# Optimization experiments

Measured on AMD Instinct MI355X. Metric: run time of the kernel, lower is better.

The kernel has to match this reference:

```python
import jax, jax.numpy as jnp
import numpy as np

N, E = 50000, 800000
F_N, F_E = 32, 16
HC, H, C, L = 128, 2, 64, 3  # hidden_channels, heads, out per head, num_layers
NEG_SLOPE = 0.2  # PyG GATConv default


def setup_inputs() -> dict:
    key = jax.random.key(0)
    ks = jax.random.split(key, 32)
    rn = lambda k, shape, s=0.05: (jax.random.normal(k, shape, jnp.float32) * s)
    return {
        "x": jax.random.normal(ks[0], (N, F_N), jnp.float32),
        "edge_index": jax.random.randint(ks[1], (2, E), 0, N),
        "edge_attr": jax.random.normal(ks[2], (E, F_E), jnp.float32),
        # node encoder: Linear(32,128) -> ReLU -> Linear(128,128)
        "w_n1": rn(ks[3], (F_N, HC)), "b_n1": jnp.zeros((HC,), jnp.float32),
        "w_n2": rn(ks[4], (HC, HC)), "b_n2": jnp.zeros((HC,), jnp.float32),
        # edge encoder: Linear(16,128) -> ReLU (output is ignored by GATConv, edge_dim=None)
        "w_e": rn(ks[5], (F_E, HC)), "b_e": jnp.zeros((HC,), jnp.float32),
        # 3 GATConv layers: lin [128,H*C], att_src/att_dst [H,C], bias [H*C]
        "conv_w": rn(ks[6], (L, HC, H * C)),
        "conv_att_src": rn(ks[7], (L, H, C)),
        "conv_att_dst": rn(ks[8], (L, H, C)),
        "conv_b": jnp.zeros((L, H * C), jnp.float32),
        # path prediction head: Linear(256,128)->ReLU->Linear(128,64)->ReLU->Linear(64,1)->Sigmoid
        "wp1": rn(ks[9], (2 * HC, HC)), "bp1": jnp.zeros((HC,), jnp.float32),
        "wp2": rn(ks[10], (HC, 64)), "bp2": jnp.zeros((64,), jnp.float32),
        "wp3": rn(ks[11], (64, 1)), "bp3": jnp.zeros((1,), jnp.float32),
        # vulnerability head: Linear(128,64)->ReLU->Linear(64,1)->Sigmoid
        "wv1": rn(ks[12], (HC, 64)), "bv1": jnp.zeros((64,), jnp.float32),
        "wv2": rn(ks[13], (64, 1)), "bv2": jnp.zeros((1,), jnp.float32),
    }


def _gat_layer(x, src, dst, w, att_src, att_dst, bias):
    n = x.shape[0]
    h = (x @ w).reshape(n, H, C)                       # [N,H,C]
    a_src = jnp.sum(h * att_src, axis=-1)              # [N,H]
    a_dst = jnp.sum(h * att_dst, axis=-1)              # [N,H]
    alpha = a_src[src] + a_dst[dst]                    # [E',H]
    alpha = jax.nn.leaky_relu(alpha, NEG_SLOPE)
    amax = jax.lax.stop_gradient(jax.ops.segment_max(alpha, dst, num_segments=n))
    ex = jnp.exp(alpha - amax[dst])
    denom = jax.ops.segment_sum(ex, dst, num_segments=n)  # [N,H] (>0: self-loops)
    coef = ex / denom[dst]                             # softmax over incoming edges
    msg = h[src] * coef[:, :, None]                    # [E',H,C]
    out = jax.ops.segment_sum(msg, dst, num_segments=n)
    return out.reshape(n, H * C) + bias


def reference(x, edge_index, edge_attr,
              w_n1, b_n1, w_n2, b_n2, w_e, b_e,
              conv_w, conv_att_src, conv_att_dst, conv_b,
              wp1, bp1, wp2, bp2, wp3, bp3, wv1, bv1, wv2, bv2):
    n = x.shape[0]
    # node encoder (dropout = identity in eval)
    h = jax.nn.relu(x @ w_n1 + b_n1) @ w_n2 + b_n2
    # edge encoder output is computed but ignored by GATConv (edge_dim=None in PyG)
    _edge_emb = jax.nn.relu(edge_attr @ w_e + b_e)
    # add self loops (GATConv default add_self_loops=True)
    loop = jnp.arange(n, dtype=edge_index.dtype)
    src = jnp.concatenate([edge_index[0], loop])
    dst = jnp.concatenate([edge_index[1], loop])
    for l in range(L):
        h = jax.nn.relu(_gat_layer(h, src, dst, conv_w[l], conv_att_src[l], conv_att_dst[l], conv_b[l]))
    g = jnp.mean(h, axis=0, keepdims=True)             # [1,128] graph embedding
    # path head on cat(x[:1], graph_embedding)
    p = jnp.concatenate([h[:1], g], axis=1)            # [1,256]
    p = jax.nn.relu(p @ wp1 + bp1)
    p = jax.nn.relu(p @ wp2 + bp2)
    path = jax.nn.sigmoid(p @ wp3 + bp3)               # [1,1]
    v = jax.nn.relu(h @ wv1 + bv1)
    vuln = jax.nn.sigmoid(v @ wv2 + bv2)               # [N,1]
    esc = jnp.zeros((1, 1), jnp.float32)               # [1,1]
    return (path, vuln, esc)
```

## Files before the change

### kernel.cpp

```cpp
#include <hip/hip_runtime.h>
#include <math.h>

#define HC 128
#define NSLOPE 0.2f

using bf16x8 = __attribute__((ext_vector_type(8))) short;
using f32x4  = __attribute__((ext_vector_type(4))) float;

__device__ __forceinline__ float lrelu(float v){ return v > 0.f ? v : NSLOPE * v; }

__device__ __forceinline__ unsigned short f2bf(float f){
    unsigned int b = __float_as_uint(f);
    b += 0x7FFFu + ((b >> 16) & 1u);
    return (unsigned short)(b >> 16);
}
__device__ __forceinline__ float bf_lo(unsigned int v){ return __uint_as_float(v << 16); }
__device__ __forceinline__ float bf_hi(unsigned int v){ return __uint_as_float(v & 0xFFFF0000u); }
__device__ __forceinline__ float bf1(unsigned short v){ return __uint_as_float((unsigned int)v << 16); }

__global__ void count_kernel(const int* __restrict__ ei, int* __restrict__ cnt,
                             int* __restrict__ rank, int E){
    int e = blockIdx.x * blockDim.x + threadIdx.x;
    if (e < E) rank[e] = atomicAdd(&cnt[ei[E + e]], 1);
}

__global__ __launch_bounds__(256) void scan_part_kernel(
        const int* __restrict__ deg, int* __restrict__ bsum, int n)
{
    int t = threadIdx.x, lane = t & 63, wid = t >> 6;
    int base = blockIdx.x * 1024 + t * 4;
    int s = 0;
    #pragma unroll
    for (int j = 0; j < 4; ++j){ int i = base + j; if (i < n) s += deg[i]; }
    #pragma unroll
    for (int o = 1; o < 64; o <<= 1) s += __shfl_xor(s, o);
    __shared__ int red[4];
    if (lane == 0) red[wid] = s;
    __syncthreads();
    if (t == 0) bsum[blockIdx.x] = red[0] + red[1] + red[2] + red[3];
}

__global__ __launch_bounds__(64) void scan_top_kernel(
        const int* __restrict__ bsum, int* __restrict__ boff, int* __restrict__ rowptr,
        int nb, int n)
{
    int t = threadIdx.x;
    int v = (t < nb) ? bsum[t] : 0;
    int incl = v;
    #pragma unroll
    for (int o = 1; o < 64; o <<= 1){ int u = __shfl_up(incl, o); if (t >= o) incl += u; }
    if (t < nb) boff[t] = incl - v;
    if (t == 63) rowptr[n] = incl;
}

__global__ __launch_bounds__(256) void scan_fin_kernel(
        const int* __restrict__ deg, const int* __restrict__ boff,
        int* __restrict__ rowptr, int n)
{
    int t = threadIdx.x, lane = t & 63, wid = t >> 6;
    int base = blockIdx.x * 1024 + t * 4;
    int d[4]; int s = 0;
    #pragma unroll
    for (int j = 0; j < 4; ++j){ int i = base + j; d[j] = (i < n) ? deg[i] : 0; s += d[j]; }
    int incl = s;
    #pragma unroll
    for (int o = 1; o < 64; o <<= 1){ int u = __shfl_up(incl, o); if (lane >= o) incl += u; }
    __shared__ int wsum[4];
    if (lane == 63) wsum[wid] = incl;
    __syncthreads();
    int off = boff[blockIdx.x] + (incl - s);
    for (int w = 0; w < wid; ++w) off += wsum[w];
    #pragma unroll
    for (int j = 0; j < 4; ++j){
        int i = base + j;
        if (i < n) rowptr[i] = off;
        off += d[j];
    }
}

__global__ __launch_bounds__(256) void scatter_kernel(
        const int* __restrict__ ei, const int* __restrict__ rowptr,
        const int* __restrict__ rank, int* __restrict__ colsrc, int E)
{
    int b = blockIdx.x * 1024 + threadIdx.x;
    int e0 = b, e1 = b + 256, e2 = b + 512, e3 = b + 768;
    bool v0 = e0 < E, v1 = e1 < E, v2 = e2 < E, v3 = e3 < E;
    int d0=0,d1=0,d2=0,d3=0, s0=0,s1=0,s2=0,s3=0, r0=0,r1=0,r2=0,r3=0;
    if (v0){ d0 = ei[E + e0]; s0 = ei[e0]; r0 = rank[e0]; }
    if (v1){ d1 = ei[E + e1]; s1 = ei[e1]; r1 = rank[e1]; }
    if (v2){ d2 = ei[E + e2]; s2 = ei[e2]; r2 = rank[e2]; }
    if (v3){ d3 = ei[E + e3]; s3 = ei[e3]; r3 = rank[e3]; }
    if (v0) colsrc[rowptr[d0] + r0] = s0;
    if (v1) colsrc[rowptr[d1] + r1] = s1;
    if (v2) colsrc[rowptr[d2] + r2] = s2;
    if (v3) colsrc[rowptr[d3] + r3] = s3;
}

__global__ __launch_bounds__(256) void wtrans_kernel(
        const float* __restrict__ W, unsigned short* __restrict__ Wt, int nmat)
{
    int idx = blockIdx.x * 256 + threadIdx.x;
    if (idx >= nmat * 2048) return;
    int mat = idx >> 11;
    int rem = idx & 2047;
    int c = rem >> 4, kg = rem & 15;
    const float* Wm = W + (size_t)mat * 16384;
    unsigned short* Wo = Wt + (size_t)mat * 16384;
    unsigned int pk[4];
    #pragma unroll
    for (int j = 0; j < 4; ++j){
        float a = Wm[(size_t)(kg*8 + j*2    ) * 128 + c];
        float b = Wm[(size_t)(kg*8 + j*2 + 1) * 128 + c];
        pk[j] = (unsigned int)f2bf(a) | ((unsigned int)f2bf(b) << 16);
    }
    *(uint4*)(Wo + (size_t)c * 128 + kg * 8) = make_uint4(pk[0], pk[1], pk[2], pk[3]);
}

__global__ __launch_bounds__(256) void enc1_kernel(
        const float* __restrict__ x, const float* __restrict__ w1, const float* __restrict__ b1,
        unsigned short* __restrict__ hid, int n)
{
    __shared__ float As[32][68];
    __shared__ float Bs[32][128];
    int t = threadIdx.x;
    int m0 = blockIdx.x * 64;
    int tm = t >> 4, tn = t & 15;

    #pragma unroll
    for (int i = 0; i < 2; ++i){
        int f = i * 256 + t;
        int row = f >> 3, kq = f & 7;
        int gr = m0 + row; if (gr > n - 1) gr = n - 1;
        float4 v = *(const float4*)(x + (size_t)gr * 32 + kq * 4);
        As[kq*4+0][row] = v.x; As[kq*4+1][row] = v.y; As[kq*4+2][row] = v.z; As[kq*4+3][row] = v.w;
    }
    #pragma unroll
    for (int i = 0; i < 4; ++i){
        int f = i * 256 + t;
        int kk = f >> 5, nq = f & 31;
        *(float4*)&Bs[kk][nq*4] = *(const float4*)(w1 + (size_t)kk * 128 + nq * 4);
    }
    __syncthreads();

    float acc[4][8];
    #pragma unroll
    for (int i = 0; i < 4; ++i)
        #pragma unroll
        for (int j = 0; j < 8; ++j) acc[i][j] = 0.f;

    #pragma unroll 4
    for (int k = 0; k < 32; ++k){
        float a[4], b[8];
        *(float4*)&a[0] = *(float4*)&As[k][tm*4];
        *(float4*)&b[0] = *(float4*)&Bs[k][tn*8];
        *(float4*)&b[4] = *(float4*)&Bs[k][tn*8+4];
        #pragma unroll
        for (int i = 0; i < 4; ++i)
            #pragma unroll
            for (int j = 0; j < 8; ++j) acc[i][j] = fmaf(a[i], b[j], acc[i][j]);
    }

    float bb[8];
    *(float4*)&bb[0] = *(const float4*)(b1 + tn*8);
    *(float4*)&bb[4] = *(const float4*)(b1 + tn*8 + 4);
    #pragma unroll
    for (int i = 0; i < 4; ++i){
        int node = m0 + tm*4 + i;
        if (node < n){
            float o[8];
            #pragma unroll
            for (int j = 0; j < 8; ++j) o[j] = fmaxf(acc[i][j] + bb[j], 0.f);
            uint4 pk;
            pk.x = (unsigned int)f2bf(o[0]) | ((unsigned int)f2bf(o[1]) << 16);
            pk.y = (unsigned int)f2bf(o[2]) | ((unsigned int)f2bf(o[3]) << 16);
            pk.z = (unsigned int)f2bf(o[4]) | ((unsigned int)f2bf(o[5]) << 16);
            pk.w = (unsigned int)f2bf(o[6]) | ((unsigned int)f2bf(o[7]) << 16);
            *(uint4*)(hid + (size_t)node*HC + tn*8) = pk;
        }
    }
}

template<bool ATT>
__global__ __launch_bounds__(256) void gemm_mfma_kernel(
        const unsigned short* __restrict__ A, const unsigned short* __restrict__ Wt,
        const float* __restrict__ bias,
        const float* __restrict__ att_s, const float* __restrict__ att_d,
        unsigned short* __restrict__ Cb,
        float* __restrict__ asrc, float* __restrict__ adst, int n)
{
    __shared__ float lds[4][16][132];
    int t = threadIdx.x;
    int w = t >> 6, l = t & 63;
    int lane15 = l & 15, lanehi = l >> 4;
    int m0 = blockIdx.x * 64 + w * 16;

    f32x4 acc[8];
    #pragma unroll
    for (int ct = 0; ct < 8; ++ct) acc[ct] = (f32x4){0.f, 0.f, 0.f, 0.f};

    int ar = m0 + lane15; if (ar > n - 1) ar = n - 1;
    const unsigned short* Arow = A + (size_t)ar * HC;

    #pragma unroll
    for (int kc = 0; kc < 4; ++kc){
        bf16x8 af = *reinterpret_cast<const bf16x8*>(Arow + kc * 32 + lanehi * 8);
        #pragma unroll
        for (int ct = 0; ct < 8; ++ct){
            bf16x8 bf = *reinterpret_cast<const bf16x8*>(
                Wt + (size_t)(ct * 16 + lane15) * HC + kc * 32 + lanehi * 8);
            acc[ct] = __builtin_amdgcn_mfma_f32_16x16x32_bf16(af, bf, acc[ct], 0, 0, 0);
        }
    }

    if (ATT){
        float ats[8], atd[8];
        #pragma unroll
        for (int ct = 0; ct < 8; ++ct){
            ats[ct] = att_s[ct * 16 + lane15];
            atd[ct] = att_d[ct * 16 + lane15];
        }
        #pragma unroll
        for (int r = 0; r < 4; ++r){
            float sa0 = 0.f, sd0 = 0.f, sa1 = 0.f, sd1 = 0.f;
            #pragma unroll
            for (int ct = 0; ct < 4; ++ct){
                sa0 = fmaf(acc[ct][r], ats[ct], sa0);
                sd0 = fmaf(acc[ct][r], atd[ct], sd0);
            }
            #pragma unroll
            for (int ct = 4; ct < 8; ++ct){
                sa1 = fmaf(acc[ct][r], ats[ct], sa1);
                sd1 = fmaf(acc[ct][r], atd[ct], sd1);
            }
            #pragma unroll
            for (int o = 1; o < 16; o <<= 1){
                sa0 += __shfl_xor(sa0, o); sd0 += __shfl_xor(sd0, o);
                sa1 += __shfl_xor(sa1, o); sd1 += __shfl_xor(sd1, o);
            }
            int node = m0 + lanehi * 4 + r;
            if (lane15 == 0 && node < n){
                asrc[(size_t)node * 2]     = sa0;
                adst[(size_t)node * 2]     = sd0;
                asrc[(size_t)node * 2 + 1] = sa1;
                adst[(size_t)node * 2 + 1] = sd1;
            }
        }
    }

    float bb[8];
    #pragma unroll
    for (int ct = 0; ct < 8; ++ct) bb[ct] = ATT ? 0.f : bias[ct * 16 + lane15];
    #pragma unroll
    for (int ct = 0; ct < 8; ++ct)
        #pragma unroll
        for (int r = 0; r < 4; ++r)
            lds[w][lanehi * 4 + r][ct * 16 + lane15] = acc[ct][r] + bb[ct];
    __syncthreads();

    int row = lane15, cb = lanehi;
    int node = m0 + row;
    if (node < n){
        #pragma unroll
        for (int q = 0; q < 4; ++q){
            float o[8];
            *(float4*)&o[0] = *(float4*)&lds[w][row][cb * 32 + q * 8];
            *(float4*)&o[4] = *(float4*)&lds[w][row][cb * 32 + q * 8 + 4];
            uint4 pk;
            pk.x = (unsigned int)f2bf(o[0]) | ((unsigned int)f2bf(o[1]) << 16);
            pk.y = (unsigned int)f2bf(o[2]) | ((unsigned int)f2bf(o[3]) << 16);
            pk.z = (unsigned int)f2bf(o[4]) | ((unsigned int)f2bf(o[5]) << 16);
            pk.w = (unsigned int)f2bf(o[6]) | ((unsigned int)f2bf(o[7]) << 16);
            *(uint4*)(Cb + (size_t)node * HC + cb * 32 + q * 8) = pk;
        }
    }
}

__global__ __launch_bounds__(64) void aggregate_kernel(
        const unsigned short* __restrict__ h1b, const float* __restrict__ asrc, const float* __restrict__ adst,
        const int* __restrict__ rowptr, const int* __restrict__ colsrc,
        const float* __restrict__ bias, unsigned short* __restrict__ hout, int n)
{
    __shared__ float4 exl[64];
    int i = blockIdx.x;
    if (i >= n) return;
    int t = threadIdx.x;
    int head = t >> 5;
    float2 adv = *(const float2*)(adst + (size_t)i * 2);
    float2 asv = *(const float2*)(asrc + (size_t)i * 2);
    float ads = head ? adv.y : adv.x;
    float exs = __expf(lrelu((head ? asv.y : asv.x) + ads));
    unsigned int hv = ((const unsigned int*)(h1b + (size_t)i * HC))[t];
    float acc0 = exs * bf_lo(hv), acc1 = exs * bf_hi(hv), D = exs;

    int e  = rowptr[i];
    int e1 = rowptr[i + 1];
    while (e < e1){
        int m = e1 - e; if (m > 64) m = 64;
        if (t < m){
            int s = colsrc[e + t];
            float2 as = *(const float2*)(asrc + (size_t)s * 2);
            exl[t] = make_float4(__int_as_float(s),
                                 __expf(lrelu(as.x + adv.x)),
                                 __expf(lrelu(as.y + adv.y)), 0.f);
        }
        __syncthreads();
        int j = 0;
        for (; j + 4 <= m; j += 4){
            float4 q0 = exl[j], q1 = exl[j+1], q2 = exl[j+2], q3 = exl[j+3];
            const unsigned int* p0 = (const unsigned int*)(h1b + (size_t)__float_as_int(q0.x) * HC);
            const unsigned int* p1 = (const unsigned int*)(h1b + (size_t)__float_as_int(q1.x) * HC);
            const unsigned int* p2 = (const unsigned int*)(h1b + (size_t)__float_as_int(q2.x) * HC);
            const unsigned int* p3 = (const unsigned int*)(h1b + (size_t)__float_as_int(q3.x) * HC);
            unsigned int v0 = p0[t], v1 = p1[t], v2 = p2[t], v3 = p3[t];
            float c0 = head ? q0.z : q0.y;
            float c1 = head ? q1.z : q1.y;
            float c2 = head ? q2.z : q2.y;
            float c3 = head ? q3.z : q3.y;
            acc0 = fmaf(c0, bf_lo(v0), acc0);  acc1 = fmaf(c0, bf_hi(v0), acc1);
            acc0 = fmaf(c1, bf_lo(v1), acc0);  acc1 = fmaf(c1, bf_hi(v1), acc1);
            acc0 = fmaf(c2, bf_lo(v2), acc0);  acc1 = fmaf(c2, bf_hi(v2), acc1);
            acc0 = fmaf(c3, bf_lo(v3), acc0);  acc1 = fmaf(c3, bf_hi(v3), acc1);
            D += (c0 + c1) + (c2 + c3);
        }
        for (; j < m; ++j){
            float4 q = exl[j];
            unsigned int v = ((const unsigned int*)(h1b + (size_t)__float_as_int(q.x) * HC))[t];
            float c = head ? q.z : q.y;
            acc0 = fmaf(c, bf_lo(v), acc0);
            acc1 = fmaf(c, bf_hi(v), acc1);
            D += c;
        }
        __syncthreads();
        e += m;
    }
    float rD = 1.0f / D;
    float o0 = fmaxf(acc0 * rD + bias[2*t],     0.f);
    float o1 = fmaxf(acc1 * rD + bias[2*t + 1], 0.f);
    ((unsigned int*)hout)[(size_t)i * 64 + t] =
        (unsigned int)f2bf(o0) | ((unsigned int)f2bf(o1) << 16);
}

__global__ __launch_bounds__(256) void mean_part_kernel(
        const unsigned short* __restrict__ h, float* __restrict__ partial, int n)
{
    int t = threadIdx.x;
    int cq = t & 31;
    int rl = t >> 5;
    float4 acc = make_float4(0.f, 0.f, 0.f, 0.f);
    for (int i = blockIdx.x * 8 + rl; i < n; i += gridDim.x * 8){
        uint2 v = *(const uint2*)(h + (size_t)i * HC + cq * 4);
        acc.x += bf_lo(v.x); acc.y += bf_hi(v.x);
        acc.z += bf_lo(v.y); acc.w += bf_hi(v.y);
    }
    __shared__ float4 red[256];
    red[t] = acc;
    __syncthreads();
    if (t < 128){
        float4 o = red[t + 128];
        red[t].x += o.x; red[t].y += o.y; red[t].z += o.z; red[t].w += o.w;
    }
    __syncthreads();
    if (t < 64){
        float4 o = red[t + 64];
        red[t].x += o.x; red[t].y += o.y; red[t].z += o.z; red[t].w += o.w;
    }
    __syncthreads();
    if (t < 32){
        float4 a = red[t], b = red[t + 32];
        float4 s = make_float4(a.x + b.x, a.y + b.y, a.z + b.z, a.w + b.w);
        *(float4*)(partial + (size_t)blockIdx.x * HC + t * 4) = s;
    }
}

__global__ __launch_bounds__(256) void mean_fin_kernel(
        const float* __restrict__ partial, float* __restrict__ g, int nb)
{
    int t = threadIdx.x;
    int cq = t & 31, b0 = t >> 5;
    float4 acc = make_float4(0.f, 0.f, 0.f, 0.f);
    for (int b = b0; b < nb; b += 8){
        float4 v = *(const float4*)(partial + (size_t)b * HC + cq * 4);
        acc.x += v.x; acc.y += v.y; acc.z += v.z; acc.w += v.w;
    }
    __shared__ float4 red[256];
    red[t] = acc;
    __syncthreads();
    if (t < 128){
        float4 o = red[t + 128];
        red[t].x += o.x; red[t].y += o.y; red[t].z += o.z; red[t].w += o.w;
    }
    __syncthreads();
    if (t < 64){
        float4 o = red[t + 64];
        red[t].x += o.x; red[t].y += o.y; red[t].z += o.z; red[t].w += o.w;
    }
    __syncthreads();
    if (t < 32){
        float4 a = red[t], b = red[t + 32];
        float4 s = make_float4(a.x + b.x, a.y + b.y, a.z + b.z, a.w + b.w);
        *(float4*)(g + t * 4) = s;
    }
}

__global__ __launch_bounds__(256) void vuln_fused_kernel(
        const unsigned short* __restrict__ h, const float* __restrict__ wv1, const float* __restrict__ bv1,
        const float* __restrict__ wv2, const float* __restrict__ bv2,
        float* __restrict__ out, int n)
{
    __shared__ float As[32][68];
    __shared__ float Bs[32][64];
    int t = threadIdx.x;
    int m0 = blockIdx.x * 64;
    int tm = t >> 4, tn = t & 15;
    int kq = t >> 6, arow = t & 63;

    float acc[4][4];
    #pragma unroll
    for (int i = 0; i < 4; ++i)
        #pragma unroll
        for (int j = 0; j < 4; ++j) acc[i][j] = 0.f;

    for (int kc = 0; kc < 4; ++kc){
        int k0 = kc * 32;
        {
            int gr = m0 + arow; if (gr > n - 1) gr = n - 1;
            uint4 v = *(const uint4*)(h + (size_t)gr * HC + k0 + kq * 8);
            As[kq*8+0][arow] = bf_lo(v.x); As[kq*8+1][arow] = bf_hi(v.x);
            As[kq*8+2][arow] = bf_lo(v.y); As[kq*8+3][arow] = bf_hi(v.y);
            As[kq*8+4][arow] = bf_lo(v.z); As[kq*8+5][arow] = bf_hi(v.z);
            As[kq*8+6][arow] = bf_lo(v.w); As[kq*8+7][arow] = bf_hi(v.w);
        }
        #pragma unroll
        for (int i = 0; i < 2; ++i){
            int f = i * 256 + t;
            int kk = f >> 4, nq = f & 15;
            *(float4*)&Bs[kk][nq*4] = *(const float4*)(wv1 + (size_t)(k0 + kk) * 64 + nq * 4);
        }
        __syncthreads();
        #pragma unroll 4
        for (int k = 0; k < 32; ++k){
            float a[4], b[4];
            *(float4*)&a[0] = *(float4*)&As[k][tm*4];
            *(float4*)&b[0] = *(float4*)&Bs[k][tn*4];
            #pragma unroll
            for (int i = 0; i < 4; ++i)
                #pragma unroll
                for (int j = 0; j < 4; ++j) acc[i][j] = fmaf(a[i], b[j], acc[i][j]);
        }
        __syncthreads();
    }

    float bb[4], wv[4];
    *(float4*)&bb[0] = *(const float4*)(bv1 + tn*4);
    *(float4*)&wv[0] = *(const float4*)(wv2 + tn*4);
    float bv2v = bv2[0];
    #pragma unroll
    for (int i = 0; i < 4; ++i){
        float v = 0.f;
        #pragma unroll
        for (int j = 0; j < 4; ++j) v = fmaf(fmaxf(acc[i][j] + bb[j], 0.f), wv[j], v);
        v += __shfl_xor(v, 1); v += __shfl_xor(v, 2);
        v += __shfl_xor(v, 4); v += __shfl_xor(v, 8);
        int node = m0 + tm*4 + i;
        if (tn == 0 && node < n)
            out[1 + node] = 1.0f / (1.0f + __expf(-(v + bv2v)));
    }
}

__global__ __launch_bounds__(128) void path_kernel(
        const unsigned short* __restrict__ h, const float* __restrict__ g,
        const float* __restrict__ wp1, const float* __restrict__ bp1,
        const float* __restrict__ wp2, const float* __restrict__ bp2,
        const float* __restrict__ wp3, const float* __restrict__ bp3,
        float* __restrict__ out, int n)
{
    __shared__ float pc[256];
    __shared__ float p1[HC];
    __shared__ float p2[64];
    int t = threadIdx.x;
    pc[t]       = bf1(h[t]);
    pc[128 + t] = g[t] * (1.0f / (float)n);
    __syncthreads();
    float a = bp1[t];
    for (int k = 0; k < 256; ++k) a = fmaf(pc[k], wp1[k * HC + t], a);
    p1[t] = fmaxf(a, 0.f);
    __syncthreads();
    if (t < 64){
        float a2 = bp2[t];
        for (int k = 0; k < HC; ++k) a2 = fmaf(p1[k], wp2[k * 64 + t], a2);
        p2[t] = fmaxf(a2, 0.f);
    }
    __syncthreads();
    if (t == 0){
        float a3 = bp3[0];
        for (int k = 0; k < 64; ++k) a3 = fmaf(p2[k], wp3[k], a3);
        out[0] = 1.0f / (1.0f + __expf(-a3));
        out[1 + n] = 0.f;
    }
}

extern "C" void kernel_launch(void* const* d_in, const int* in_sizes, int n_in,
                              void* d_out, int out_size, void* d_ws, size_t ws_size,
                              hipStream_t stream)
{
    const float* x    = (const float*)d_in[0];
    const int*   ei   = (const int*)d_in[1];
    const float* w_n1 = (const float*)d_in[3];
    const float* b_n1 = (const float*)d_in[4];
    const float* w_n2 = (const float*)d_in[5];
    const float* b_n2 = (const float*)d_in[6];
    const float* conv_w = (const float*)d_in[9];
    const float* att_s  = (const float*)d_in[10];
    const float* att_d  = (const float*)d_in[11];
    const float* conv_b = (const float*)d_in[12];
    const float* wp1 = (const float*)d_in[13];
    const float* bp1 = (const float*)d_in[14];
    const float* wp2 = (const float*)d_in[15];
    const float* bp2 = (const float*)d_in[16];
    const float* wp3 = (const float*)d_in[17];
    const float* bp3 = (const float*)d_in[18];
    const float* wv1 = (const float*)d_in[19];
    const float* bv1 = (const float*)d_in[20];
    const float* wv2 = (const float*)d_in[21];
    const float* bv2 = (const float*)d_in[22];

    const int N = in_sizes[0] / 32;
    const int E = in_sizes[1] / 2;
    float* out = (float*)d_out;

    char* ws = (char*)d_ws;
    size_t off = 0;
    auto take = [&](size_t bytes) -> char* {
        char* p = ws + off;
        off += (bytes + 255) & ~(size_t)255;
        return p;
    };
    unsigned short* hA = (unsigned short*)take((size_t)N * HC * 2);
    unsigned short* hB = (unsigned short*)take((size_t)N * HC * 2);
    float* asrc  = (float*)take((size_t)N * 2 * 4);
    float* adst  = (float*)take((size_t)N * 2 * 4);
    int*   rowptr= (int*)take((size_t)(N + 1) * 4);
    int*   cnt   = (int*)take((size_t)N * 4);
    int*   rank  = (int*)take((size_t)E * 4);
    int*   colsrc= (int*)take((size_t)E * 4);
    float* g     = (float*)take(HC * 4);
    unsigned short* Wt0 = (unsigned short*)take(16384 * 2);
    unsigned short* Wt1 = (unsigned short*)take((size_t)3 * 16384 * 2);
    const int MB = 64;
    float* mpart = (float*)take((size_t)MB * HC * 4);
    int nb = (N + 1023) / 1024;
    int*   bsum  = (int*)take((size_t)((nb + 63) & ~63) * 4);
    int*   boff  = (int*)take((size_t)((nb + 63) & ~63) * 4);

    hipMemsetAsync(cnt, 0, (size_t)N * 4, stream);
    count_kernel<<<(E + 255) / 256, 256, 0, stream>>>(ei, cnt, rank, E);
    scan_part_kernel<<<nb, 256, 0, stream>>>(cnt, bsum, N);
    scan_top_kernel<<<1, 64, 0, stream>>>(bsum, boff, rowptr, nb, N);
    scan_fin_kernel<<<nb, 256, 0, stream>>>(cnt, boff, rowptr, N);
    scatter_kernel<<<(E + 1023) / 1024, 256, 0, stream>>>(ei, rowptr, rank, colsrc, E);

    wtrans_kernel<<<8, 256, 0, stream>>>(w_n2, Wt0, 1);
    wtrans_kernel<<<24, 256, 0, stream>>>(conv_w, Wt1, 3);

    int nblk64 = (N + 63) / 64;
    enc1_kernel<<<nblk64, 256, 0, stream>>>(x, w_n1, b_n1, hB, N);
    gemm_mfma_kernel<false><<<nblk64, 256, 0, stream>>>(
        hB, Wt0, b_n2, nullptr, nullptr, hA, nullptr, nullptr, N);

    for (int l = 0; l < 3; ++l){
        gemm_mfma_kernel<true><<<nblk64, 256, 0, stream>>>(
            hA, Wt1 + (size_t)l * 16384, nullptr,
            att_s + (size_t)l * HC, att_d + (size_t)l * HC,
            hB, asrc, adst, N);
        aggregate_kernel<<<N, 64, 0, stream>>>(
            hB, asrc, adst, rowptr, colsrc, conv_b + (size_t)l * HC, hA, N);
    }

    mean_part_kernel<<<MB, 256, 0, stream>>>(hA, mpart, N);
    mean_fin_kernel<<<1, 256, 0, stream>>>(mpart, g, MB);
    vuln_fused_kernel<<<nblk64, 256, 0, stream>>>(hA, wv1, bv1, wv2, bv2, out, N);
    path_kernel<<<1, 128, 0, stream>>>(hA, g, wp1, bp1, wp2, bp2, wp3, bp3, out, N);
}
```

Before: 336.8 us.

## Use MFMA for vulnerability head and widen unrolling in scatter and aggregate

```diff
diff --git a/kernel.cpp b/kernel.cpp
--- a/kernel.cpp
+++ b/kernel.cpp
@@ -82,38 +82,37 @@
         const int* __restrict__ ei, const int* __restrict__ rowptr,
         const int* __restrict__ rank, int* __restrict__ colsrc, int E)
 {
-    int b = blockIdx.x * 1024 + threadIdx.x;
-    int e0 = b, e1 = b + 256, e2 = b + 512, e3 = b + 768;
-    bool v0 = e0 < E, v1 = e1 < E, v2 = e2 < E, v3 = e3 < E;
-    int d0=0,d1=0,d2=0,d3=0, s0=0,s1=0,s2=0,s3=0, r0=0,r1=0,r2=0,r3=0;
-    if (v0){ d0 = ei[E + e0]; s0 = ei[e0]; r0 = rank[e0]; }
-    if (v1){ d1 = ei[E + e1]; s1 = ei[e1]; r1 = rank[e1]; }
-    if (v2){ d2 = ei[E + e2]; s2 = ei[e2]; r2 = rank[e2]; }
-    if (v3){ d3 = ei[E + e3]; s3 = ei[e3]; r3 = rank[e3]; }
-    if (v0) colsrc[rowptr[d0] + r0] = s0;
-    if (v1) colsrc[rowptr[d1] + r1] = s1;
-    if (v2) colsrc[rowptr[d2] + r2] = s2;
-    if (v3) colsrc[rowptr[d3] + r3] = s3;
+    int b = blockIdx.x * 2048 + threadIdx.x;
+    int e[8]; bool v[8]; int d[8], s[8], r[8];
+    #pragma unroll
+    for (int i = 0; i < 8; ++i){ e[i] = b + i * 256; v[i] = e[i] < E; }
+    #pragma unroll
+    for (int i = 0; i < 8; ++i) if (v[i]){ d[i] = ei[E + e[i]]; s[i] = ei[e[i]]; r[i] = rank[e[i]]; }
+    #pragma unroll
+    for (int i = 0; i < 8; ++i) if (v[i]) colsrc[rowptr[d[i]] + r[i]] = s[i];
 }
 
 __global__ __launch_bounds__(256) void wtrans_kernel(
-        const float* __restrict__ W, unsigned short* __restrict__ Wt, int nmat)
-{
+        const float* __restrict__ W, unsigned short* __restrict__ Wt,
+        int K, int C, int nmat)
+{
+    int kg8 = K >> 3;
+    int per = C * kg8;
     int idx = blockIdx.x * 256 + threadIdx.x;
-    if (idx >= nmat * 2048) return;
-    int mat = idx >> 11;
-    int rem = idx & 2047;
-    int c = rem >> 4, kg = rem & 15;
-    const float* Wm = W + (size_t)mat * 16384;
-    unsigned short* Wo = Wt + (size_t)mat * 16384;
+    if (idx >= nmat * per) return;
+    int mat = idx / per;
+    int rem = idx - mat * per;
+    int c = rem / kg8, kg = rem - c * kg8;
+    const float* Wm = W + (size_t)mat * K * C;
+    unsigned short* Wo = Wt + (size_t)mat * K * C;
     unsigned int pk[4];
     #pragma unroll
     for (int j = 0; j < 4; ++j){
-        float a = Wm[(size_t)(kg*8 + j*2    ) * 128 + c];
-        float b = Wm[(size_t)(kg*8 + j*2 + 1) * 128 + c];
+        float a = Wm[(size_t)(kg*8 + j*2    ) * C + c];
+        float b = Wm[(size_t)(kg*8 + j*2 + 1) * C + c];
         pk[j] = (unsigned int)f2bf(a) | ((unsigned int)f2bf(b) << 16);
     }
-    *(uint4*)(Wo + (size_t)c * 128 + kg * 8) = make_uint4(pk[0], pk[1], pk[2], pk[3]);
+    *(uint4*)(Wo + (size_t)c * K + kg * 8) = make_uint4(pk[0], pk[1], pk[2], pk[3]);
 }
 
 __global__ __launch_bounds__(256) void enc1_kernel(
@@ -305,22 +304,21 @@
         }
         __syncthreads();
         int j = 0;
-        for (; j + 4 <= m; j += 4){
-            float4 q0 = exl[j], q1 = exl[j+1], q2 = exl[j+2], q3 = exl[j+3];
-            const unsigned int* p0 = (const unsigned int*)(h1b + (size_t)__float_as_int(q0.x) * HC);
-            const unsigned int* p1 = (const unsigned int*)(h1b + (size_t)__float_as_int(q1.x) * HC);
-            const unsigned int* p2 = (const unsigned int*)(h1b + (size_t)__float_as_int(q2.x) * HC);
-            const unsigned int* p3 = (const unsigned int*)(h1b + (size_t)__float_as_int(q3.x) * HC);
-            unsigned int v0 = p0[t], v1 = p1[t], v2 = p2[t], v3 = p3[t];
-            float c0 = head ? q0.z : q0.y;
-            float c1 = head ? q1.z : q1.y;
-            float c2 = head ? q2.z : q2.y;
-            float c3 = head ? q3.z : q3.y;
-            acc0 = fmaf(c0, bf_lo(v0), acc0);  acc1 = fmaf(c0, bf_hi(v0), acc1);
-            acc0 = fmaf(c1, bf_lo(v1), acc0);  acc1 = fmaf(c1, bf_hi(v1), acc1);
-            acc0 = fmaf(c2, bf_lo(v2), acc0);  acc1 = fmaf(c2, bf_hi(v2), acc1);
-            acc0 = fmaf(c3, bf_lo(v3), acc0);  acc1 = fmaf(c3, bf_hi(v3), acc1);
-            D += (c0 + c1) + (c2 + c3);
+        for (; j + 8 <= m; j += 8){
+            float4 q[8];
+            #pragma unroll
+            for (int u = 0; u < 8; ++u) q[u] = exl[j + u];
+            unsigned int v[8];
+            #pragma unroll
+            for (int u = 0; u < 8; ++u)
+                v[u] = ((const unsigned int*)(h1b + (size_t)__float_as_int(q[u].x) * HC))[t];
+            #pragma unroll
+            for (int u = 0; u < 8; ++u){
+                float c = head ? q[u].z : q[u].y;
+                acc0 = fmaf(c, bf_lo(v[u]), acc0);
+                acc1 = fmaf(c, bf_hi(v[u]), acc1);
+                D += c;
+            }
         }
         for (; j < m; ++j){
             float4 q = exl[j];
@@ -402,68 +400,52 @@
     }
 }
 
-__global__ __launch_bounds__(256) void vuln_fused_kernel(
-        const unsigned short* __restrict__ h, const float* __restrict__ wv1, const float* __restrict__ bv1,
-        const float* __restrict__ wv2, const float* __restrict__ bv2,
-        float* __restrict__ out, int n)
-{
-    __shared__ float As[32][68];
-    __shared__ float Bs[32][64];
-    int t = threadIdx.x;
-    int m0 = blockIdx.x * 64;
-    int tm = t >> 4, tn = t & 15;
-    int kq = t >> 6, arow = t & 63;
-
-    float acc[4][4];
-    #pragma unroll
-    for (int i = 0; i < 4; ++i)
-        #pragma unroll
-        for (int j = 0; j < 4; ++j) acc[i][j] = 0.f;
-
+__global__ __launch_bounds__(256) void vuln_mfma_kernel(
+        const unsigned short* __restrict__ h, const unsigned short* __restrict__ Wtv,
+        const float* __restrict__ bv1, const float* __restrict__ wv2,
+        const float* __restrict__ bv2, float* __restrict__ out, int n)
+{
+    int t = threadIdx.x;
+    int w = t >> 6, l = t & 63;
+    int lane15 = l & 15, lanehi = l >> 4;
+    int m0 = blockIdx.x * 64 + w * 16;
+
+    f32x4 acc[4];
+    #pragma unroll
+    for (int ct = 0; ct < 4; ++ct) acc[ct] = (f32x4){0.f, 0.f, 0.f, 0.f};
+
+    int ar = m0 + lane15; if (ar > n - 1) ar = n - 1;
+    const unsigned short* Arow = h + (size_t)ar * HC;
+
+    #pragma unroll
     for (int kc = 0; kc < 4; ++kc){
-        int k0 = kc * 32;
-        {
-            int gr = m0 + arow; if (gr > n - 1) gr = n - 1;
-            uint4 v = *(const uint4*)(h + (size_t)gr * HC + k0 + kq * 8);
-            As[kq*8+0][arow] = bf_lo(v.x); As[kq*8+1][arow] = bf_hi(v.x);
-            As[kq*8+2][arow] = bf_lo(v.y); As[kq*8+3][arow] = bf_hi(v.y);
-            As[kq*8+4][arow] = bf_lo(v.z); As[kq*8+5][arow] = bf_hi(v.z);
-            As[kq*8+6][arow] = bf_lo(v.w); As[kq*8+7][arow] = bf_hi(v.w);
-        }
-        #pragma unroll
-        for (int i = 0; i < 2; ++i){
-            int f = i * 256 + t;
-            int kk = f >> 4, nq = f & 15;
-            *(float4*)&Bs[kk][nq*4] = *(const float4*)(wv1 + (size_t)(k0 + kk) * 64 + nq * 4);
-        }
-        __syncthreads();
-        #pragma unroll 4
-        for (int k = 0; k < 32; ++k){
-            float a[4], b[4];
-            *(float4*)&a[0] = *(float4*)&As[k][tm*4];
-            *(float4*)&b[0] = *(float4*)&Bs[k][tn*4];
-            #pragma unroll
-            for (int i = 0; i < 4; ++i)
-                #pragma unroll
-                for (int j = 0; j < 4; ++j) acc[i][j] = fmaf(a[i], b[j], acc[i][j]);
-        }
-        __syncthreads();
+        bf16x8 af = *reinterpret_cast<const bf16x8*>(Arow + kc * 32 + lanehi * 8);
+        #pragma unroll
+        for (int ct = 0; ct < 4; ++ct){
+            bf16x8 bf = *reinterpret_cast<const bf16x8*>(
+                Wtv + (size_t)(ct * 16 + lane15) * HC + kc * 32 + lanehi * 8);
+            acc[ct] = __builtin_amdgcn_mfma_f32_16x16x32_bf16(af, bf, acc[ct], 0, 0, 0);
+        }
     }
 
     float bb[4], wv[4];
-    *(float4*)&bb[0] = *(const float4*)(bv1 + tn*4);
-    *(float4*)&wv[0] = *(const float4*)(wv2 + tn*4);
+    #pragma unroll
+    for (int ct = 0; ct < 4; ++ct){
+        bb[ct] = bv1[ct * 16 + lane15];
+        wv[ct] = wv2[ct * 16 + lane15];
+    }
     float bv2v = bv2[0];
     #pragma unroll
-    for (int i = 0; i < 4; ++i){
-        float v = 0.f;
-        #pragma unroll
-        for (int j = 0; j < 4; ++j) v = fmaf(fmaxf(acc[i][j] + bb[j], 0.f), wv[j], v);
-        v += __shfl_xor(v, 1); v += __shfl_xor(v, 2);
-        v += __shfl_xor(v, 4); v += __shfl_xor(v, 8);
-        int node = m0 + tm*4 + i;
-        if (tn == 0 && node < n)
-            out[1 + node] = 1.0f / (1.0f + __expf(-(v + bv2v)));
+    for (int r = 0; r < 4; ++r){
+        float s = 0.f;
+        #pragma unroll
+        for (int ct = 0; ct < 4; ++ct)
+            s = fmaf(fmaxf(acc[ct][r] + bb[ct], 0.f), wv[ct], s);
+        #pragma unroll
+        for (int o = 1; o < 16; o <<= 1) s += __shfl_xor(s, o);
+        int node = m0 + lanehi * 4 + r;
+        if (lane15 == 0 && node < n)
+            out[1 + node] = 1.0f / (1.0f + __expf(-(s + bv2v)));
     }
 }
 
@@ -546,6 +528,7 @@
     float* g     = (float*)take(HC * 4);
     unsigned short* Wt0 = (unsigned short*)take(16384 * 2);
     unsigned short* Wt1 = (unsigned short*)take((size_t)3 * 16384 * 2);
+    unsigned short* Wtv = (unsigned short*)take(8192 * 2);
     const int MB = 64;
     float* mpart = (float*)take((size_t)MB * HC * 4);
     int nb = (N + 1023) / 1024;
@@ -557,10 +540,11 @@
     scan_part_kernel<<<nb, 256, 0, stream>>>(cnt, bsum, N);
     scan_top_kernel<<<1, 64, 0, stream>>>(bsum, boff, rowptr, nb, N);
     scan_fin_kernel<<<nb, 256, 0, stream>>>(cnt, boff, rowptr, N);
-    scatter_kernel<<<(E + 1023) / 1024, 256, 0, stream>>>(ei, rowptr, rank, colsrc, E);
-
-    wtrans_kernel<<<8, 256, 0, stream>>>(w_n2, Wt0, 1);
-    wtrans_kernel<<<24, 256, 0, stream>>>(conv_w, Wt1, 3);
+    scatter_kernel<<<(E + 2047) / 2048, 256, 0, stream>>>(ei, rowptr, rank, colsrc, E);
+
+    wtrans_kernel<<<8, 256, 0, stream>>>(w_n2, Wt0, 128, 128, 1);
+    wtrans_kernel<<<24, 256, 0, stream>>>(conv_w, Wt1, 128, 128, 3);
+    wtrans_kernel<<<4, 256, 0, stream>>>(wv1, Wtv, 128, 64, 1);
 
     int nblk64 = (N + 63) / 64;
     enc1_kernel<<<nblk64, 256, 0, stream>>>(x, w_n1, b_n1, hB, N);
@@ -578,6 +562,6 @@
 
     mean_part_kernel<<<MB, 256, 0, stream>>>(hA, mpart, N);
     mean_fin_kernel<<<1, 256, 0, stream>>>(mpart, g, MB);
-    vuln_fused_kernel<<<nblk64, 256, 0, stream>>>(hA, wv1, bv1, wv2, bv2, out, N);
+    vuln_mfma_kernel<<<nblk64, 256, 0, stream>>>(hA, Wtv, bv1, wv2, bv2, out, N);
     path_kernel<<<1, 128, 0, stream>>>(hA, g, wp1, bp1, wp2, bp2, wp3, bp3, out, N);
 }
```

Measured after the change: 333.9 us. Within noise of the previous version (-0.9%).
